# Kernel tuning notes

Hardware: AMD Instinct MI355X
Metric: run time of the kernel (lower is better)

The kernel has to match this reference:

```python
import jax, jax.numpy as jnp
import numpy as np

D_MODEL = 768
NUM_HEADS = 12
D_K = D_MODEL // NUM_HEADS


def setup_inputs() -> dict:
    key = jax.random.key(0)
    ks = jax.random.split(key, 9)
    B, S = 2, 4096
    s = 1.0 / np.sqrt(D_MODEL).astype(np.float32)
    inp = {
        "x": jax.random.normal(ks[0], (B, S, D_MODEL), dtype=jnp.float32),
        "wq": jax.random.normal(ks[1], (D_MODEL, D_MODEL), dtype=jnp.float32) * s,
        "bq": jnp.zeros((D_MODEL,), dtype=jnp.float32),
        "wk": jax.random.normal(ks[2], (D_MODEL, D_MODEL), dtype=jnp.float32) * s,
        "bk": jnp.zeros((D_MODEL,), dtype=jnp.float32),
        "wv": jax.random.normal(ks[3], (D_MODEL, D_MODEL), dtype=jnp.float32) * s,
        "bv": jnp.zeros((D_MODEL,), dtype=jnp.float32),
        "wo": jax.random.normal(ks[4], (D_MODEL, D_MODEL), dtype=jnp.float32) * s,
        "bo": jnp.zeros((D_MODEL,), dtype=jnp.float32),
    }
    return inp


def reference(x, wq, bq, wk, bk, wv, bv, wo, bo):
    B, S, D = x.shape
    H, dk = NUM_HEADS, D_K
    # projections (torch Linear: x @ W^T + b); weights here stored as [in, out]
    def proj(w, b):
        y = jnp.einsum("bsd,df->bsf", x, w) + b
        return y.reshape(B, S, H, dk).transpose(0, 2, 1, 3)  # [B,H,S,dk]
    q = proj(wq, bq)
    k = proj(wk, bk)
    v = proj(wv, bv)
    scores = jnp.einsum("bhqd,bhkd->bhqk", q, k) / np.sqrt(dk).astype(np.float32)
    attn = jax.nn.softmax(scores, axis=-1)  # dropout is identity in eval
    out = jnp.einsum("bhqk,bhkd->bhqd", attn, v)
    out = out.transpose(0, 2, 1, 3).reshape(B, S, D)
    return jnp.einsum("bsd,df->bsf", out, wo) + bo
```

## Files before the change

kernel.cpp:

```cpp
#include <hip/hip_runtime.h>

typedef unsigned short u16;
typedef unsigned int u32;
typedef __bf16 bf16x8 __attribute__((ext_vector_type(8)));
typedef short s16x4 __attribute__((ext_vector_type(4)));
typedef float f32x4 __attribute__((ext_vector_type(4)));

#define AS1(p) ((const __attribute__((address_space(1))) void*)(p))
#define AS3(p) ((__attribute__((address_space(3))) void*)(p))

#if __has_builtin(__builtin_amdgcn_exp2f)
#define EXP2(x) __builtin_amdgcn_exp2f(x)
#else
#define EXP2(x) __builtin_exp2f(x)
#endif

__device__ __forceinline__ u16 f2bf(float f) {
    u32 u = __float_as_uint(f);
    u += 0x7fffu + ((u >> 16) & 1u);
    return (u16)(u >> 16);
}

__device__ __forceinline__ short bfbits(float f) {
    __bf16 h = (__bf16)f;
    return __builtin_bit_cast(short, h);
}

#define NXQ 6291456
#define QSCALE 0.1803368801111249f

__global__ __launch_bounds__(256) void prep_kernel(
    const float* __restrict__ x,
    const float* __restrict__ wq, const float* __restrict__ wk,
    const float* __restrict__ wv, const float* __restrict__ wo,
    const float* __restrict__ bq, const float* __restrict__ bk,
    const float* __restrict__ bv,
    u16* __restrict__ xbf, u16* __restrict__ WT, float* __restrict__ bqkv)
{
    const int t = threadIdx.x;
    const int bid = blockIdx.x;
    if (bid < 6144) {
        int i = bid * 256 + t;
        float4 v = ((const float4*)x)[i];
        uint2 o;
        o.x = (u32)f2bf(v.x) | ((u32)f2bf(v.y) << 16);
        o.y = (u32)f2bf(v.z) | ((u32)f2bf(v.w) << 16);
        ((uint2*)xbf)[i] = o;
        return;
    }
    int tb = bid - 6144;
    int mat = tb / 144;
    int tt = tb - mat * 144;
    int tr = tt / 12, tc = tt - tr * 12;
    const float* W = (mat == 0) ? wq : (mat == 1) ? wk : (mat == 2) ? wv : wo;
    __shared__ u16 sT[64 * 72];
    #pragma unroll
    for (int rr = 0; rr < 4; ++rr) {
        int r = (t >> 4) + rr * 16;
        int cb = (t & 15) * 4;
        float4 v = *(const float4*)&W[(size_t)(tr * 64 + r) * 768 + tc * 64 + cb];
        sT[(cb + 0) * 72 + r] = f2bf(v.x);
        sT[(cb + 1) * 72 + r] = f2bf(v.y);
        sT[(cb + 2) * 72 + r] = f2bf(v.z);
        sT[(cb + 3) * 72 + r] = f2bf(v.w);
    }
    __syncthreads();
    #pragma unroll
    for (int i = 0; i < 2; ++i) {
        int nr = t >> 2;
        int cc = (t & 3) * 16 + i * 8;
        *(uint4*)&WT[(size_t)(mat * 768 + tc * 64 + nr) * 768 + tr * 64 + cc] =
            *(uint4*)&sT[nr * 72 + cc];
    }
    if (tb < 9) {
        int i = tb * 256 + t;
        if (i < 2304)
            bqkv[i] = (i < 768) ? bq[i] : (i < 1536) ? bk[i - 768] : bv[i - 1536];
    }
}

template<int MODE>
__global__ __launch_bounds__(256, 4) void gemm_kernel(
    const u16* __restrict__ A, const u16* __restrict__ WT,
    const float* __restrict__ bias, void* __restrict__ out)
{
    __shared__ u16 sA[128 * 64];
    __shared__ u16 sB[128 * 64];

    const int m0 = blockIdx.x * 128;
    const int n0g = blockIdx.y * 128;
    const int tid = threadIdx.x, lane = tid & 63, wave = tid >> 6;
    const int quad = lane >> 4, l16 = lane & 15;
    const int wm = (wave & 1) * 64, wn = (wave >> 1) * 64;

    f32x4 acc[4][4];
    #pragma unroll
    for (int i = 0; i < 4; ++i)
        #pragma unroll
        for (int j = 0; j < 4; ++j)
            #pragma unroll
            for (int r = 0; r < 4; ++r)
                acc[i][j][r] = 0.f;

    const int srow = (lane >> 3);

    for (int k0 = 0; k0 < 768; k0 += 64) {
        __syncthreads();
        #pragma unroll
        for (int i = 0; i < 4; ++i) {
            int c = wave * 4 + i;
            int row = c * 8 + srow;
            __builtin_amdgcn_global_load_lds(
                AS1(&A[(size_t)(m0 + row) * 768 + k0 + (((lane & 7) ^ (row & 7)) * 8)]),
                AS3(&sA[c * 512]), 16, 0, 0);
            __builtin_amdgcn_global_load_lds(
                AS1(&WT[(size_t)(n0g + row) * 768 + k0 + (((lane & 7) ^ (row & 7)) * 8)]),
                AS3(&sB[c * 512]), 16, 0, 0);
        }
        __syncthreads();
        #pragma unroll
        for (int s = 0; s < 2; ++s) {
            bf16x8 af[4], bfr[4];
            #pragma unroll
            for (int i = 0; i < 4; ++i) {
                int row = wm + i * 16 + l16;
                af[i] = *(const bf16x8*)&sA[row * 64 + (((s * 4 + quad) ^ (row & 7)) * 8)];
            }
            #pragma unroll
            for (int j = 0; j < 4; ++j) {
                int row = wn + j * 16 + l16;
                bfr[j] = *(const bf16x8*)&sB[row * 64 + (((s * 4 + quad) ^ (row & 7)) * 8)];
            }
            #pragma unroll
            for (int i = 0; i < 4; ++i)
                #pragma unroll
                for (int j = 0; j < 4; ++j)
                    acc[i][j] = __builtin_amdgcn_mfma_f32_16x16x32_bf16(af[i], bfr[j], acc[i][j], 0, 0, 0);
        }
    }

    if (MODE == 0) {
        const int mat = blockIdx.y / 6;
        const int nm0 = n0g - mat * 768;
        const float scale = (mat == 0) ? QSCALE : 1.0f;
        u16* dst = (u16*)out + (size_t)mat * NXQ;
        #pragma unroll
        for (int i = 0; i < 4; ++i) {
            #pragma unroll
            for (int j = 0; j < 4; ++j) {
                int colg = n0g + wn + j * 16 + l16;
                int col = nm0 + wn + j * 16 + l16;
                float bv = bias[colg];
                int h = col >> 6, d = col & 63;
                int row0 = m0 + wm + i * 16 + quad * 4;
                int b = row0 >> 12, s = row0 & 4095;
                if (mat < 2) {
                    #pragma unroll
                    for (int r = 0; r < 4; ++r)
                        dst[(((size_t)(b * 12 + h) * 4096) + s + r) * 64 + d] =
                            f2bf((acc[i][j][r] + bv) * scale);
                } else {
                    ushort4 w;
                    w.x = f2bf(acc[i][j][0] + bv);
                    w.y = f2bf(acc[i][j][1] + bv);
                    w.z = f2bf(acc[i][j][2] + bv);
                    w.w = f2bf(acc[i][j][3] + bv);
                    *(ushort4*)&dst[(((size_t)(b * 12 + h) * 64 + d) * 4096) + s] = w;
                }
            }
        }
    } else {
        #pragma unroll
        for (int i = 0; i < 4; ++i) {
            #pragma unroll
            for (int j = 0; j < 4; ++j) {
                int col = n0g + wn + j * 16 + l16;
                float bv = bias[col];
                #pragma unroll
                for (int r = 0; r < 4; ++r) {
                    int row = m0 + wm + i * 16 + quad * 4 + r;
                    ((float*)out)[(size_t)row * 768 + col] = acc[i][j][r] + bv;
                }
            }
        }
    }
}

__global__ __launch_bounds__(256, 2) void flash_kernel(
    const u16* __restrict__ Q, const u16* __restrict__ K,
    const u16* __restrict__ Vt, u16* __restrict__ O)
{
    const int bh = blockIdx.y;
    const int q0 = blockIdx.x * 128;
    const u16* Qp = Q + (size_t)bh * 4096 * 64;
    const u16* Kp = K + (size_t)bh * 4096 * 64;
    const u16* Vp = Vt + (size_t)bh * 64 * 4096;
    const int tid = threadIdx.x, lane = tid & 63, wave = tid >> 6;
    const int quad = lane >> 4, l16 = lane & 15;

    __shared__ u16 sK[2][64 * 64];
    __shared__ u16 sVT[2][64 * 64];
    __shared__ u16 sP[4][32 * 72];

    const int qrow = q0 + wave * 32;
    bf16x8 qf[2][2];
    #pragma unroll
    for (int i = 0; i < 2; ++i)
        #pragma unroll
        for (int s = 0; s < 2; ++s)
            qf[i][s] = *(const bf16x8*)&Qp[(size_t)(qrow + i * 16 + l16) * 64 + s * 32 + quad * 8];

    f32x4 oacc[4][2];
    f32x4 lacc[2];
    #pragma unroll
    for (int jd = 0; jd < 4; ++jd)
        #pragma unroll
        for (int i = 0; i < 2; ++i)
            #pragma unroll
            for (int r = 0; r < 4; ++r)
                oacc[jd][i][r] = 0.f;
    #pragma unroll
    for (int i = 0; i < 2; ++i)
        #pragma unroll
        for (int r = 0; r < 4; ++r)
            lacc[i][r] = 0.f;

    bf16x8 ones;
    #pragma unroll
    for (int r = 0; r < 8; ++r) ones[r] = (__bf16)1.0f;

    u16* sPw = &sP[wave][0];

    const int srow = lane >> 3;
    auto stage = [&](int t, int buf) {
        #pragma unroll
        for (int i = 0; i < 2; ++i) {
            int c = wave * 2 + i;
            int row = c * 8 + srow;
            int kc = ((lane & 7) ^ (row & 7)) * 8;
            __builtin_amdgcn_global_load_lds(
                AS1(&Kp[(size_t)(t * 64 + row) * 64 + kc]),
                AS3(&sK[buf][c * 512]), 16, 0, 0);
            __builtin_amdgcn_global_load_lds(
                AS1(&Vp[(size_t)row * 4096 + t * 64 + kc]),
                AS3(&sVT[buf][c * 512]), 16, 0, 0);
        }
    };

    auto body = [&](int cur) {
        f32x4 sacc[4][2];
        #pragma unroll
        for (int m = 0; m < 4; ++m)
            #pragma unroll
            for (int i = 0; i < 2; ++i)
                #pragma unroll
                for (int r = 0; r < 4; ++r)
                    sacc[m][i][r] = 0.f;
        #pragma unroll
        for (int s = 0; s < 2; ++s) {
            bf16x8 ak[4];
            #pragma unroll
            for (int m = 0; m < 4; ++m) {
                int row = m * 16 + l16;
                ak[m] = *(const bf16x8*)&sK[cur][row * 64 + (((s * 4 + quad) ^ (row & 7)) * 8)];
            }
            #pragma unroll
            for (int m = 0; m < 4; ++m)
                #pragma unroll
                for (int i = 0; i < 2; ++i)
                    sacc[m][i] = __builtin_amdgcn_mfma_f32_16x16x32_bf16(ak[m], qf[i][s], sacc[m][i], 0, 0, 0);
        }

        #pragma unroll
        for (int i = 0; i < 2; ++i) {
            #pragma unroll
            for (int kk = 0; kk < 4; ++kk) {
                s16x4 b;
                b[0] = bfbits(EXP2(sacc[kk][i][0]));
                b[1] = bfbits(EXP2(sacc[kk][i][1]));
                b[2] = bfbits(EXP2(sacc[kk][i][2]));
                b[3] = bfbits(EXP2(sacc[kk][i][3]));
                *(s16x4*)&sPw[(i * 16 + l16) * 72 + kk * 16 + quad * 4] = b;
            }
        }

        #pragma unroll
        for (int kb = 0; kb < 2; ++kb) {
            bf16x8 av[4], pb[2];
            #pragma unroll
            for (int jd = 0; jd < 4; ++jd) {
                int row = jd * 16 + l16;
                av[jd] = *(const bf16x8*)&sVT[cur][row * 64 + (((kb * 4 + quad) ^ (row & 7)) * 8)];
            }
            #pragma unroll
            for (int i = 0; i < 2; ++i)
                pb[i] = *(const bf16x8*)&sPw[(i * 16 + l16) * 72 + kb * 32 + quad * 8];
            #pragma unroll
            for (int i = 0; i < 2; ++i) {
                #pragma unroll
                for (int jd = 0; jd < 4; ++jd)
                    oacc[jd][i] = __builtin_amdgcn_mfma_f32_16x16x32_bf16(av[jd], pb[i], oacc[jd][i], 0, 0, 0);
                lacc[i] = __builtin_amdgcn_mfma_f32_16x16x32_bf16(ones, pb[i], lacc[i], 0, 0, 0);
            }
        }
    };

    stage(0, 0);
    for (int t = 0; t < 64; t += 2) {
        __syncthreads();
        stage(t + 1, 1);
        body(0);
        __syncthreads();
        if (t + 2 < 64) stage(t + 2, 0);
        body(1);
    }

    const int b = bh / 12, h = bh - b * 12;
    #pragma unroll
    for (int i = 0; i < 2; ++i) {
        float inv = 1.0f / lacc[i][0];
        int s = qrow + i * 16 + l16;
        #pragma unroll
        for (int jd = 0; jd < 4; ++jd) {
            ushort4 w;
            w.x = f2bf(oacc[jd][i][0] * inv);
            w.y = f2bf(oacc[jd][i][1] * inv);
            w.z = f2bf(oacc[jd][i][2] * inv);
            w.w = f2bf(oacc[jd][i][3] * inv);
            *(ushort4*)&O[((size_t)(b * 4096 + s)) * 768 + h * 64 + jd * 16 + quad * 4] = w;
        }
    }
}

extern "C" void kernel_launch(void* const* d_in, const int* in_sizes, int n_in,
                              void* d_out, int out_size, void* d_ws, size_t ws_size,
                              hipStream_t stream)
{
    (void)in_sizes; (void)n_in; (void)out_size; (void)ws_size;
    const float* x  = (const float*)d_in[0];
    const float* wq = (const float*)d_in[1];
    const float* bq = (const float*)d_in[2];
    const float* wk = (const float*)d_in[3];
    const float* bk = (const float*)d_in[4];
    const float* wv = (const float*)d_in[5];
    const float* bv = (const float*)d_in[6];
    const float* wo = (const float*)d_in[7];
    const float* bo = (const float*)d_in[8];
    float* out = (float*)d_out;

    u16* ws = (u16*)d_ws;
    u16* xbf = ws;
    u16* WT  = xbf + (size_t)8192 * 768;
    u16* Qb  = WT + (size_t)3072 * 768;
    u16* Kb  = Qb + NXQ;
    u16* Vtb = Kb + NXQ;
    u16* Ob  = Vtb + NXQ;
    float* bqkv = (float*)(Ob + NXQ);

    prep_kernel<<<6720, 256, 0, stream>>>(x, wq, wk, wv, wo, bq, bk, bv, xbf, WT, bqkv);
    gemm_kernel<0><<<dim3(64, 18), 256, 0, stream>>>(xbf, WT, bqkv, Qb);
    flash_kernel<<<dim3(32, 24), 256, 0, stream>>>(Qb, Kb, Vtb, Ob);
    gemm_kernel<1><<<dim3(64, 6), 256, 0, stream>>>(Ob, WT + (size_t)2304 * 768, bo, out);
}
```

Baseline: 275.8 us.

## Switch flash attention to 32x32 MFMA with in-register P via permlane swap

Rewrites the attention inner loop to use 32x32x16 bf16 MFMA tiles, keeping the softmax probabilities in registers and rearranging them with v_permlane32_swap instead of a round trip through shared memory. The row-sum is accumulated with scalar adds plus one cross-half shuffle, replacing the extra MFMA against a ones vector. It also adds s_setprio around the MFMA sections and raises the occupancy hint to 3 blocks per SM. The aim is to cut LDS traffic and instruction count, at the cost of register pressure and reliance on gfx950-specific instructions.

```diff
diff --git a/kernel.cpp b/kernel.cpp
--- a/kernel.cpp
+++ b/kernel.cpp
@@ -3,8 +3,9 @@
 typedef unsigned short u16;
 typedef unsigned int u32;
 typedef __bf16 bf16x8 __attribute__((ext_vector_type(8)));
-typedef short s16x4 __attribute__((ext_vector_type(4)));
 typedef float f32x4 __attribute__((ext_vector_type(4)));
+typedef float f32x16 __attribute__((ext_vector_type(16)));
+typedef int i32x4 __attribute__((ext_vector_type(4)));
 
 #define AS1(p) ((const __attribute__((address_space(1))) void*)(p))
 #define AS3(p) ((__attribute__((address_space(3))) void*)(p))
@@ -21,9 +22,10 @@
     return (u16)(u >> 16);
 }
 
-__device__ __forceinline__ short bfbits(float f) {
-    __bf16 h = (__bf16)f;
-    return __builtin_bit_cast(short, h);
+__device__ __forceinline__ int cvt_pk_bf16(float lo, float hi) {
+    int r;
+    asm("v_cvt_pk_bf16_f32 %0, %1, %2" : "=v"(r) : "v"(lo), "v"(hi));
+    return r;
 }
 
 #define NXQ 6291456
@@ -186,7 +188,7 @@
     }
 }
 
-__global__ __launch_bounds__(256, 2) void flash_kernel(
+__global__ __launch_bounds__(256, 3) void flash_kernel(
     const u16* __restrict__ Q, const u16* __restrict__ K,
     const u16* __restrict__ Vt, u16* __restrict__ O)
 {
@@ -196,40 +198,24 @@
     const u16* Kp = K + (size_t)bh * 4096 * 64;
     const u16* Vp = Vt + (size_t)bh * 64 * 4096;
     const int tid = threadIdx.x, lane = tid & 63, wave = tid >> 6;
-    const int quad = lane >> 4, l16 = lane & 15;
+    const int l32 = lane & 31, hf = lane >> 5;
 
     __shared__ u16 sK[2][64 * 64];
     __shared__ u16 sVT[2][64 * 64];
-    __shared__ u16 sP[4][32 * 72];
 
     const int qrow = q0 + wave * 32;
-    bf16x8 qf[2][2];
-    #pragma unroll
-    for (int i = 0; i < 2; ++i)
-        #pragma unroll
-        for (int s = 0; s < 2; ++s)
-            qf[i][s] = *(const bf16x8*)&Qp[(size_t)(qrow + i * 16 + l16) * 64 + s * 32 + quad * 8];
-
-    f32x4 oacc[4][2];
-    f32x4 lacc[2];
-    #pragma unroll
-    for (int jd = 0; jd < 4; ++jd)
-        #pragma unroll
-        for (int i = 0; i < 2; ++i)
-            #pragma unroll
-            for (int r = 0; r < 4; ++r)
-                oacc[jd][i][r] = 0.f;
-    #pragma unroll
-    for (int i = 0; i < 2; ++i)
-        #pragma unroll
-        for (int r = 0; r < 4; ++r)
-            lacc[i][r] = 0.f;
-
-    bf16x8 ones;
-    #pragma unroll
-    for (int r = 0; r < 8; ++r) ones[r] = (__bf16)1.0f;
-
-    u16* sPw = &sP[wave][0];
+    bf16x8 qf[4];
+    #pragma unroll
+    for (int k16 = 0; k16 < 4; ++k16)
+        qf[k16] = *(const bf16x8*)&Qp[(size_t)(qrow + l32) * 64 + k16 * 16 + hf * 8];
+
+    f32x16 oacc[2];
+    #pragma unroll
+    for (int dt = 0; dt < 2; ++dt)
+        #pragma unroll
+        for (int r = 0; r < 16; ++r)
+            oacc[dt][r] = 0.f;
+    float lpart = 0.f;
 
     const int srow = lane >> 3;
     auto stage = [&](int t, int buf) {
@@ -248,61 +234,63 @@
     };
 
     auto body = [&](int cur) {
-        f32x4 sacc[4][2];
-        #pragma unroll
-        for (int m = 0; m < 4; ++m)
-            #pragma unroll
-            for (int i = 0; i < 2; ++i)
-                #pragma unroll
-                for (int r = 0; r < 4; ++r)
-                    sacc[m][i][r] = 0.f;
-        #pragma unroll
-        for (int s = 0; s < 2; ++s) {
-            bf16x8 ak[4];
-            #pragma unroll
-            for (int m = 0; m < 4; ++m) {
-                int row = m * 16 + l16;
-                ak[m] = *(const bf16x8*)&sK[cur][row * 64 + (((s * 4 + quad) ^ (row & 7)) * 8)];
-            }
-            #pragma unroll
-            for (int m = 0; m < 4; ++m)
-                #pragma unroll
-                for (int i = 0; i < 2; ++i)
-                    sacc[m][i] = __builtin_amdgcn_mfma_f32_16x16x32_bf16(ak[m], qf[i][s], sacc[m][i], 0, 0, 0);
-        }
-
-        #pragma unroll
-        for (int i = 0; i < 2; ++i) {
-            #pragma unroll
-            for (int kk = 0; kk < 4; ++kk) {
-                s16x4 b;
-                b[0] = bfbits(EXP2(sacc[kk][i][0]));
-                b[1] = bfbits(EXP2(sacc[kk][i][1]));
-                b[2] = bfbits(EXP2(sacc[kk][i][2]));
-                b[3] = bfbits(EXP2(sacc[kk][i][3]));
-                *(s16x4*)&sPw[(i * 16 + l16) * 72 + kk * 16 + quad * 4] = b;
-            }
-        }
-
-        #pragma unroll
-        for (int kb = 0; kb < 2; ++kb) {
-            bf16x8 av[4], pb[2];
-            #pragma unroll
-            for (int jd = 0; jd < 4; ++jd) {
-                int row = jd * 16 + l16;
-                av[jd] = *(const bf16x8*)&sVT[cur][row * 64 + (((kb * 4 + quad) ^ (row & 7)) * 8)];
-            }
-            #pragma unroll
-            for (int i = 0; i < 2; ++i)
-                pb[i] = *(const bf16x8*)&sPw[(i * 16 + l16) * 72 + kb * 32 + quad * 8];
-            #pragma unroll
-            for (int i = 0; i < 2; ++i) {
-                #pragma unroll
-                for (int jd = 0; jd < 4; ++jd)
-                    oacc[jd][i] = __builtin_amdgcn_mfma_f32_16x16x32_bf16(av[jd], pb[i], oacc[jd][i], 0, 0, 0);
-                lacc[i] = __builtin_amdgcn_mfma_f32_16x16x32_bf16(ones, pb[i], lacc[i], 0, 0, 0);
-            }
-        }
+        f32x16 sacc[2];
+        #pragma unroll
+        for (int kt = 0; kt < 2; ++kt)
+            #pragma unroll
+            for (int r = 0; r < 16; ++r)
+                sacc[kt][r] = 0.f;
+        __builtin_amdgcn_s_setprio(1);
+        #pragma unroll
+        for (int kt = 0; kt < 2; ++kt) {
+            #pragma unroll
+            for (int k16 = 0; k16 < 4; ++k16) {
+                int row = kt * 32 + l32;
+                bf16x8 ak = *(const bf16x8*)&sK[cur][row * 64 + (((k16 * 2 + hf) ^ (row & 7)) * 8)];
+                sacc[kt] = __builtin_amdgcn_mfma_f32_32x32x16_bf16(ak, qf[k16], sacc[kt], 0, 0, 0);
+            }
+        }
+        __builtin_amdgcn_s_setprio(0);
+
+        int W[2][4][2];
+        #pragma unroll
+        for (int kt = 0; kt < 2; ++kt) {
+            float p[16];
+            #pragma unroll
+            for (int r = 0; r < 16; ++r) p[r] = EXP2(sacc[kt][r]);
+            lpart += (((p[0] + p[1]) + (p[2] + p[3])) + ((p[4] + p[5]) + (p[6] + p[7])))
+                   + (((p[8] + p[9]) + (p[10] + p[11])) + ((p[12] + p[13]) + (p[14] + p[15])));
+            #pragma unroll
+            for (int g = 0; g < 4; ++g) {
+                W[kt][g][0] = cvt_pk_bf16(p[g * 4 + 0], p[g * 4 + 1]);
+                W[kt][g][1] = cvt_pk_bf16(p[g * 4 + 2], p[g * 4 + 3]);
+            }
+        }
+
+        bf16x8 pf[4];
+        #pragma unroll
+        for (int ks = 0; ks < 4; ++ks) {
+            int kt = ks >> 1, gA = (ks & 1) * 2;
+            int a0 = W[kt][gA][0], b0 = W[kt][gA + 1][0];
+            int a1 = W[kt][gA][1], b1 = W[kt][gA + 1][1];
+            asm("v_permlane32_swap_b32 %0, %1" : "+v"(a0), "+v"(b0));
+            asm("v_permlane32_swap_b32 %0, %1" : "+v"(a1), "+v"(b1));
+            i32x4 t4;
+            t4[0] = a0; t4[1] = a1; t4[2] = b0; t4[3] = b1;
+            pf[ks] = __builtin_bit_cast(bf16x8, t4);
+        }
+
+        __builtin_amdgcn_s_setprio(1);
+        #pragma unroll
+        for (int dt = 0; dt < 2; ++dt) {
+            #pragma unroll
+            for (int ks = 0; ks < 4; ++ks) {
+                int row = dt * 32 + l32;
+                bf16x8 av = *(const bf16x8*)&sVT[cur][row * 64 + (((ks * 2 + hf) ^ (row & 7)) * 8)];
+                oacc[dt] = __builtin_amdgcn_mfma_f32_32x32x16_bf16(av, pf[ks], oacc[dt], 0, 0, 0);
+            }
+        }
+        __builtin_amdgcn_s_setprio(0);
     };
 
     stage(0, 0);
@@ -315,19 +303,21 @@
         body(1);
     }
 
-    const int b = bh / 12, h = bh - b * 12;
-    #pragma unroll
-    for (int i = 0; i < 2; ++i) {
-        float inv = 1.0f / lacc[i][0];
-        int s = qrow + i * 16 + l16;
-        #pragma unroll
-        for (int jd = 0; jd < 4; ++jd) {
+    float lfull = lpart + __shfl_xor(lpart, 32, 64);
+    float inv = 1.0f / lfull;
+    const int b = bh / 12, hh = bh - b * 12;
+    const int token = qrow + l32;
+    u16* Obase = O + ((size_t)(b * 4096 + token)) * 768 + hh * 64;
+    #pragma unroll
+    for (int dt = 0; dt < 2; ++dt) {
+        #pragma unroll
+        for (int g = 0; g < 4; ++g) {
             ushort4 w;
-            w.x = f2bf(oacc[jd][i][0] * inv);
-            w.y = f2bf(oacc[jd][i][1] * inv);
-            w.z = f2bf(oacc[jd][i][2] * inv);
-            w.w = f2bf(oacc[jd][i][3] * inv);
-            *(ushort4*)&O[((size_t)(b * 4096 + s)) * 768 + h * 64 + jd * 16 + quad * 4] = w;
+            w.x = f2bf(oacc[dt][g * 4 + 0] * inv);
+            w.y = f2bf(oacc[dt][g * 4 + 1] * inv);
+            w.z = f2bf(oacc[dt][g * 4 + 2] * inv);
+            w.w = f2bf(oacc[dt][g * 4 + 3] * inv);
+            *(ushort4*)&Obase[dt * 32 + g * 8 + hf * 4] = w;
         }
     }
 }
```

New measurement: 265.8 us. 3.6% less time.
